# Kernel optimization log

Hardware: AMD Instinct MI355X
Metric: run time of the kernel (lower is better)

The kernel has to match this reference:

```python
import jax, jax.numpy as jnp
import numpy as np
from jax import lax

# --- geometry constants (match init_kwargs geo) ---
NVOX = (128, 128, 128)          # (nz, ny, nx) voxels
SVOX = (256.0, 256.0, 256.0)    # volume size in mm
NDET = (256, 256)               # (V, U) detector pixels
SDET = (512.0, 512.0)           # detector size in mm
DSO = 1000.0                    # source-to-isocenter distance
DSD = 1536.0                    # source-to-detector distance
N_ANGLES = 360


def setup_inputs() -> dict:
    key = jax.random.key(0)
    # projections: [B, 1, n_angles, nDetV, nDetU]
    x = jax.random.normal(key, (2, 1, N_ANGLES, NDET[0], NDET[1]), dtype=jnp.float32)
    return {"x": x}


def _backproject(proj):
    """Voxel-driven cone-beam back-projection (adjoint of cone-beam forward projector).

    proj: [B, A, V, U] projections over a circular source trajectory.
    returns volume [B, nz, ny, nx].
    """
    B, A, V, U = proj.shape
    nz, ny, nx = NVOX
    dz, dy, dx = SVOX[0] / nz, SVOX[1] / ny, SVOX[2] / nx
    dv, du = SDET[0] / V, SDET[1] / U

    # voxel center coordinates (isocenter at origin)
    zc = ((jnp.arange(nz, dtype=jnp.float32) - (nz - 1) / 2) * dz)[:, None, None]  # [nz,1,1]
    yc = ((jnp.arange(ny, dtype=jnp.float32) - (ny - 1) / 2) * dy)[None, :, None]  # [1,ny,1]
    xc = ((jnp.arange(nx, dtype=jnp.float32) - (nx - 1) / 2) * dx)[None, None, :]  # [1,1,nx]

    angles = jnp.linspace(0.0, 2.0 * np.pi, A, endpoint=False, dtype=jnp.float32)
    proj_a = jnp.moveaxis(proj, 1, 0)  # [A, B, V, U] for scan over angles

    def bilinear(p, iv, iu):
        # p: [B, V, U]; iv, iu: [nz, ny, nx] fractional detector coords
        valid = (iu >= 0) & (iu <= U - 1) & (iv >= 0) & (iv <= V - 1)
        iu = jnp.clip(iu, 0.0, U - 1.0)
        iv = jnp.clip(iv, 0.0, V - 1.0)
        u0 = jnp.floor(iu).astype(jnp.int32)
        v0 = jnp.floor(iv).astype(jnp.int32)
        u1 = jnp.minimum(u0 + 1, U - 1)
        v1 = jnp.minimum(v0 + 1, V - 1)
        fu = iu - u0
        fv = iv - v0
        s = (p[:, v0, u0] * ((1 - fv) * (1 - fu))
             + p[:, v0, u1] * ((1 - fv) * fu)
             + p[:, v1, u0] * (fv * (1 - fu))
             + p[:, v1, u1] * (fv * fu))            # [B,nz,ny,nx]
        return s * valid.astype(p.dtype)

    def body(vol, inp):
        theta, p = inp                                # scalar, [B,V,U]
        c, s = jnp.cos(theta), jnp.sin(theta)
        xr = xc * c + yc * s                          # rotated in-plane coords [1,ny,nx]
        yr = -xc * s + yc * c                         # [1,ny,nx]
        mag = DSD / (DSO - xr)                        # perspective magnification [1,ny,nx]
        iu = jnp.broadcast_to(yr * mag / du + (U - 1) / 2, (nz, ny, nx))
        iv = zc * mag / dv + (V - 1) / 2              # [nz,ny,nx]
        vol = vol + bilinear(p, iv, iu)
        return vol, None

    vol0 = jnp.zeros((B, nz, ny, nx), dtype=proj.dtype)
    vol, _ = lax.scan(body, vol0, (angles, proj_a))
    return vol


def reference(x):
    # x: [B, 1, A, V, U] -> volume [B, 1, nz, ny, nx]
    vol = _backproject(x[:, 0])
    return vol[:, None]
```

## Files before the change

kernel.cpp:

```cpp
#include <hip/hip_runtime.h>
#include <math.h>

#define NA   360
#define ZPT  8
#define ROWS 24
#define COLS 52
#define NSTG 1280
#define PITCHB (COLS*4)


typedef __attribute__((address_space(1))) const void gas_t;
typedef __attribute__((address_space(3))) void las_t;

__device__ __forceinline__ int2 bbox_angle(float c, float s,
    float xclo, float xchi, float yclo, float ychi, float zvlo, float zvhi)
{
    const float a0 = xclo*c, a1 = xchi*c, b0 = yclo*s, b1 = ychi*s;
    const float xr0 = a0+b0, xr1 = a0+b1, xr2 = a1+b0, xr3 = a1+b1;
    const float xmn = fminf(fminf(xr0,xr1), fminf(xr2,xr3));
    const float xmx = fmaxf(fmaxf(xr0,xr1), fmaxf(xr2,xr3));
    const float c0 = yclo*c, c1 = ychi*c, d0 = xclo*s, d1 = xchi*s;
    const float yr0 = c0-d0, yr1 = c0-d1, yr2 = c1-d0, yr3 = c1-d1;
    const float ymn = fminf(fminf(yr0,yr1), fminf(yr2,yr3));
    const float ymx = fmaxf(fmaxf(yr0,yr1), fmaxf(yr2,yr3));
    const float mlo = 1536.f * __builtin_amdgcn_rcpf(1000.f - xmn);
    const float mhi = 1536.f * __builtin_amdgcn_rcpf(1000.f - xmx);
    const float umn = fminf(fminf(ymn*mlo, ymn*mhi), fminf(ymx*mlo, ymx*mhi));
    int u_lo = (int)floorf(fmaf(umn, 0.5f, 127.5f)) - 1;
    u_lo = u_lo < 0 ? 0 : (u_lo > 256-COLS ? 256-COLS : u_lo);
    const float vmn = fminf(fminf(zvlo*mlo, zvlo*mhi), fminf(zvhi*mlo, zvhi*mhi));
    int v_lo = (int)floorf(vmn + 127.5f) - 1;
    v_lo = v_lo < 0 ? 0 : (v_lo > 231 ? 231 : v_lo);
    return make_int2(u_lo, v_lo);
}

__device__ __forceinline__ void stage5(const float* g, float* lds_wave,
                                       const int goffB[5]) {
    #pragma unroll
    for (int i = 0; i < 5; ++i) {
        __builtin_amdgcn_global_load_lds(
            (gas_t*)((const char*)g + goffB[i]),
            (las_t*)(lds_wave + i * 256),
            4, 0, 0);
    }
}

__device__ __forceinline__ void compute_angle(const float* __restrict__ smb,
    float c, float s, float xc, float yc, float zf0, int u_lo, int v_lo,
    float acc[ZPT])
{
    const float xr  = xc*c + yc*s;
    const float yr  = yc*c - xc*s;
    const float mag = 1536.f * __builtin_amdgcn_rcpf(1000.f - xr);
    const float iu  = fmaf(yr*mag, 0.5f, 127.5f);
    const bool uval = (iu >= 0.f) && (iu <= 255.f);
    const float iuc = fminf(fmaxf(iu, 0.f), 255.f);
    int u0 = (int)iuc; u0 = u0 > 254 ? 254 : u0;
    const float fu  = iuc - (float)u0;
    const float w   = uval ? 1.f : 0.f;
    const float wu1 = fu*w, wu0 = w - wu1;
    const int   ub  = (u0 - u_lo) << 2;
    const float ivb = fmaf(zf0, mag, 127.5f) - (float)v_lo;
    #pragma unroll
    for (int k = 0; k < ZPT; ++k) {
        const float ivl = fmaf((float)k, mag, ivb);
        const int   v0  = (int)ivl;
        const float fv  = ivl - (float)v0;
        const char* p   = (const char*)smb + (v0*PITCHB + ub);
        const float p00 = *(const float*)p;
        const float p01 = *(const float*)(p + 4);
        const float p10 = *(const float*)(p + PITCHB);
        const float p11 = *(const float*)(p + PITCHB + 4);
        const float q0 = fmaf(fv, p10 - p00, p00);
        const float q1 = fmaf(fv, p11 - p01, p01);
        acc[k] = fmaf(wu0, q0, acc[k]);
        acc[k] = fmaf(wu1, q1, acc[k]);
    }
}

__global__ __launch_bounds__(256, 4) void bp_kernel(const float* __restrict__ proj,
                                                    float* __restrict__ out) {
    __shared__ float2 cs_sh[NA];
    __shared__ int2   bb_sh[NA];
    __shared__ float  patch[2][NSTG];

    const int tid = threadIdx.y * 16 + threadIdx.x;

    const int zg = blockIdx.x;
    const int t  = blockIdx.y;
    const int b  = blockIdx.z;
    const int x0 = (t & 7) * 16;
    const int y0 = (t >> 3) * 16;
    const int zb = zg * ZPT;

    const float zf0  = (float)zb - 63.5f;
    const float xclo = ((float)x0 - 63.5f) * 2.f, xchi = xclo + 30.f;
    const float yclo = ((float)y0 - 63.5f) * 2.f, ychi = yclo + 30.f;

    for (int i = tid; i < NA; i += 256) {
        float th = (float)i * (float)(2.0 * M_PI / (double)NA);
        float sv, cv; sincosf(th, &sv, &cv);
        cs_sh[i] = make_float2(cv, sv);
        bb_sh[i] = bbox_angle(cv, sv, xclo, xchi, yclo, ychi, zf0, zf0 + 7.f);
    }
    __syncthreads();

    int goffB[5];
    #pragma unroll
    for (int i = 0; i < 5; ++i) {
        const int flat = tid + 256 * i;
        const int r  = (flat * 1261) >> 16;
        const int cc = flat - r * 52;
        goffB[i] = (r * 256 + cc) * 4;
    }

    const float* projB = proj + (size_t)b * (NA * 65536);
    const float xc = ((float)(x0 + threadIdx.x) - 63.5f) * 2.f;
    const float yc = ((float)(y0 + threadIdx.y) - 63.5f) * 2.f;

    float* wv0 = &patch[0][tid & 192];
    float* wv1 = &patch[1][tid & 192];

    float acc[ZPT];
    #pragma unroll
    for (int k = 0; k < ZPT; ++k) acc[k] = 0.f;

    {
        const int2 lo = bb_sh[0];
        stage5(projB + (lo.y << 8) + lo.x, wv0, goffB);
    }
    __syncthreads();

    for (int a = 0; a < NA; a += 2) {
        {
            const int2 lo = bb_sh[a + 1];
            stage5(projB + (a + 1) * 65536 + (lo.y << 8) + lo.x, wv1, goffB);
        }
        {
            const float2 cs = cs_sh[a];
            const int2   lo = bb_sh[a];
            compute_angle(patch[0], cs.x, cs.y, xc, yc, zf0, lo.x, lo.y, acc);
        }
        __syncthreads();
        if (a + 2 < NA) {
            const int2 lo = bb_sh[a + 2];
            stage5(projB + (a + 2) * 65536 + (lo.y << 8) + lo.x, wv0, goffB);
        }
        {
            const float2 cs = cs_sh[a + 1];
            const int2   lo = bb_sh[a + 1];
            compute_angle(patch[1], cs.x, cs.y, xc, yc, zf0, lo.x, lo.y, acc);
        }
        __syncthreads();
    }

    float* o = out + (((size_t)b * 128 + zb) * 128 + (y0 + threadIdx.y)) * 128
                   + (x0 + threadIdx.x);
    #pragma unroll
    for (int k = 0; k < ZPT; ++k) {
        o[(size_t)k * (128 * 128)] = acc[k];
    }
}

extern "C" void kernel_launch(void* const* d_in, const int* in_sizes, int n_in,
                              void* d_out, int out_size, void* d_ws, size_t ws_size,
                              hipStream_t stream) {
    const float* proj = (const float*)d_in[0];
    float* out = (float*)d_out;
    dim3 grid(128 / ZPT, 64, 2);
    dim3 block(16, 16, 1);
    hipLaunchKernelGGL(bp_kernel, grid, block, 0, stream, proj, out);
}
```

Before: 847.5 us.

## Stage projection patches with 16-byte LDS loads and pack bilinear math

Each per-angle detector patch grows from 24x52 to 32x64 floats with a power-of-two pitch. It is now staged with two 16-byte global_load_lds instructions per lane, using wave-uniform base offsets, instead of five 4-byte ones. The bilinear interpolation and accumulation are rewritten with two-wide float vectors so the compiler can use packed FMAs, with the two halves summed at the end. The aim is to cut load-issue and VALU instruction count, in exchange for more staged bytes per angle and a larger LDS footprint.

```diff
diff --git a/kernel.cpp b/kernel.cpp
--- a/kernel.cpp
+++ b/kernel.cpp
@@ -1,14 +1,16 @@
 #include <hip/hip_runtime.h>
 #include <math.h>
 
-#define NA   360
-#define ZPT  8
-#define ROWS 24
-#define COLS 52
-#define NSTG 1280
-#define PITCHB (COLS*4)
+#define NA    360
+#define ZPT   8
+#define PROWS 32
+#define PCOLS 64
+#define NSTG  (PROWS*PCOLS)
+#define VLO_MAX 224
+#define ULO_MAX 192
 
 
+typedef float v2f __attribute__((ext_vector_type(2)));
 typedef __attribute__((address_space(1))) const void gas_t;
 typedef __attribute__((address_space(3))) void las_t;
 
@@ -27,27 +29,22 @@
     const float mhi = 1536.f * __builtin_amdgcn_rcpf(1000.f - xmx);
     const float umn = fminf(fminf(ymn*mlo, ymn*mhi), fminf(ymx*mlo, ymx*mhi));
     int u_lo = (int)floorf(fmaf(umn, 0.5f, 127.5f)) - 1;
-    u_lo = u_lo < 0 ? 0 : (u_lo > 256-COLS ? 256-COLS : u_lo);
+    u_lo = u_lo < 0 ? 0 : (u_lo > ULO_MAX ? ULO_MAX : u_lo);
     const float vmn = fminf(fminf(zvlo*mlo, zvlo*mhi), fminf(zvhi*mlo, zvhi*mhi));
     int v_lo = (int)floorf(vmn + 127.5f) - 1;
-    v_lo = v_lo < 0 ? 0 : (v_lo > 231 ? 231 : v_lo);
+    v_lo = v_lo < 0 ? 0 : (v_lo > VLO_MAX ? VLO_MAX : v_lo);
     return make_int2(u_lo, v_lo);
 }
 
-__device__ __forceinline__ void stage5(const float* g, float* lds_wave,
-                                       const int goffB[5]) {
-    #pragma unroll
-    for (int i = 0; i < 5; ++i) {
-        __builtin_amdgcn_global_load_lds(
-            (gas_t*)((const char*)g + goffB[i]),
-            (las_t*)(lds_wave + i * 256),
-            4, 0, 0);
-    }
+__device__ __forceinline__ void stage2(const char* gb, int vb0, int vb1,
+                                       float* l0, float* l1) {
+    __builtin_amdgcn_global_load_lds((gas_t*)(gb + vb0), (las_t*)l0, 16, 0, 0);
+    __builtin_amdgcn_global_load_lds((gas_t*)(gb + vb1), (las_t*)l1, 16, 0, 0);
 }
 
 __device__ __forceinline__ void compute_angle(const float* __restrict__ smb,
     float c, float s, float xc, float yc, float zf0, int u_lo, int v_lo,
-    float acc[ZPT])
+    v2f acc[ZPT])
 {
     const float xr  = xc*c + yc*s;
     const float yr  = yc*c - xc*s;
@@ -59,22 +56,20 @@
     const float fu  = iuc - (float)u0;
     const float w   = uval ? 1.f : 0.f;
     const float wu1 = fu*w, wu0 = w - wu1;
-    const int   ub  = (u0 - u_lo) << 2;
+    const v2f   wuv = {wu0, wu1};
+    const int   ui  = u0 - u_lo;
     const float ivb = fmaf(zf0, mag, 127.5f) - (float)v_lo;
     #pragma unroll
     for (int k = 0; k < ZPT; ++k) {
         const float ivl = fmaf((float)k, mag, ivb);
         const int   v0  = (int)ivl;
         const float fv  = ivl - (float)v0;
-        const char* p   = (const char*)smb + (v0*PITCHB + ub);
-        const float p00 = *(const float*)p;
-        const float p01 = *(const float*)(p + 4);
-        const float p10 = *(const float*)(p + PITCHB);
-        const float p11 = *(const float*)(p + PITCHB + 4);
-        const float q0 = fmaf(fv, p10 - p00, p00);
-        const float q1 = fmaf(fv, p11 - p01, p01);
-        acc[k] = fmaf(wu0, q0, acc[k]);
-        acc[k] = fmaf(wu1, q1, acc[k]);
+        const float* r  = smb + ((v0 << 6) + ui);
+        v2f p0 = {r[0],  r[1]};
+        v2f p1 = {r[64], r[65]};
+        const v2f fvv = {fv, fv};
+        const v2f q = __builtin_elementwise_fma(fvv, p1 - p0, p0);
+        acc[k] = __builtin_elementwise_fma(wuv, q, acc[k]);
     }
 }
 
@@ -105,36 +100,38 @@
     }
     __syncthreads();
 
-    int goffB[5];
-    #pragma unroll
-    for (int i = 0; i < 5; ++i) {
-        const int flat = tid + 256 * i;
-        const int r  = (flat * 1261) >> 16;
-        const int cc = flat - r * 52;
-        goffB[i] = (r * 256 + cc) * 4;
-    }
+    const int lane = tid & 63;
+    const int vb0  = ((lane >> 4) * 256 + (lane & 15) * 4) * 4;
+    const int vb1  = vb0 + 4096;
+    const uint32_t wslab = __builtin_amdgcn_readfirstlane((uint32_t)(tid >> 6) * 8192u);
 
-    const float* projB = proj + (size_t)b * (NA * 65536);
+    const char* projB = (const char*)(proj + (size_t)b * (NA * 65536));
     const float xc = ((float)(x0 + threadIdx.x) - 63.5f) * 2.f;
     const float yc = ((float)(y0 + threadIdx.y) - 63.5f) * 2.f;
 
-    float* wv0 = &patch[0][tid & 192];
-    float* wv1 = &patch[1][tid & 192];
+    float* l0a = &patch[0][(tid >> 6) * 512];
+    float* l0b = l0a + 256;
+    float* l1a = &patch[1][(tid >> 6) * 512];
+    float* l1b = l1a + 256;
 
-    float acc[ZPT];
+    v2f acc[ZPT];
     #pragma unroll
-    for (int k = 0; k < ZPT; ++k) acc[k] = 0.f;
+    for (int k = 0; k < ZPT; ++k) acc[k] = (v2f){0.f, 0.f};
 
     {
         const int2 lo = bb_sh[0];
-        stage5(projB + (lo.y << 8) + lo.x, wv0, goffB);
+        const uint32_t boff = __builtin_amdgcn_readfirstlane(
+            ((uint32_t)lo.y << 10) + ((uint32_t)lo.x << 2));
+        stage2(projB + (boff + wslab), vb0, vb1, l0a, l0b);
     }
     __syncthreads();
 
     for (int a = 0; a < NA; a += 2) {
         {
             const int2 lo = bb_sh[a + 1];
-            stage5(projB + (a + 1) * 65536 + (lo.y << 8) + lo.x, wv1, goffB);
+            const uint32_t boff = __builtin_amdgcn_readfirstlane(
+                ((uint32_t)lo.y << 10) + ((uint32_t)lo.x << 2));
+            stage2(projB + ((uint32_t)(a + 1) * 262144u + boff + wslab), vb0, vb1, l1a, l1b);
         }
         {
             const float2 cs = cs_sh[a];
@@ -144,7 +141,9 @@
         __syncthreads();
         if (a + 2 < NA) {
             const int2 lo = bb_sh[a + 2];
-            stage5(projB + (a + 2) * 65536 + (lo.y << 8) + lo.x, wv0, goffB);
+            const uint32_t boff = __builtin_amdgcn_readfirstlane(
+                ((uint32_t)lo.y << 10) + ((uint32_t)lo.x << 2));
+            stage2(projB + ((uint32_t)(a + 2) * 262144u + boff + wslab), vb0, vb1, l0a, l0b);
         }
         {
             const float2 cs = cs_sh[a + 1];
@@ -158,7 +157,7 @@
                    + (x0 + threadIdx.x);
     #pragma unroll
     for (int k = 0; k < ZPT; ++k) {
-        o[(size_t)k * (128 * 128)] = acc[k];
+        o[(size_t)k * (128 * 128)] = acc[k].x + acc[k].y;
     }
 }
 
```

Result: faster. 814.6 us (-3.9%).
